# Optimization experiments

Measured on AMD Instinct MI355X. Metric: run time of the kernel, lower is better.

Reference implementation:

```python
import jax, jax.numpy as jnp
import numpy as np

B, Q, PAST, MAXC = 2, 1024, 1024, 4096
H, HKV, D, HID = 32, 8, 128, 4096
HALF = D // 2
GROUPS = H // HKV
EPS = 1e-6
SCALE = 1.0 / (D ** 0.5)


def setup_inputs() -> dict:
    key = jax.random.key(0)
    ks = jax.random.split(key, 6)
    hidden_states = jax.random.normal(ks[0], (B, Q, HID), jnp.float32)
    k_cache = jax.random.normal(ks[1], (B, HKV, MAXC, D), jnp.float32)
    v_cache = jax.random.normal(ks[2], (B, HKV, MAXC, D), jnp.float32)
    # rope table: [1, max_pos, head_dim], cos in first half, sin in second half
    inv_freq = 1.0 / (10000.0 ** (jnp.arange(0, HALF, dtype=jnp.float32) / HALF))
    ang = jnp.arange(MAXC, dtype=jnp.float32)[:, None] * inv_freq[None, :]
    rope_rotary_cos_sin = jnp.concatenate([jnp.cos(ang), jnp.sin(ang)], axis=-1)[None]
    context_lengths = jnp.full((B,), Q, dtype=jnp.int32)
    kvcache_start_index = jnp.full((B,), PAST, dtype=jnp.int32)
    w_qkv = jax.random.normal(ks[3], (HID, (H + 2 * HKV) * D), jnp.float32) * 0.02
    w_o = jax.random.normal(ks[4], (HKV * D, HID), jnp.float32) * 0.02
    q_norm_w = jnp.ones((D,), jnp.float32)
    k_norm_w = jnp.ones((D,), jnp.float32)
    return dict(hidden_states=hidden_states, k_cache=k_cache, v_cache=v_cache,
                rope_rotary_cos_sin=rope_rotary_cos_sin,
                context_lengths=context_lengths,
                kvcache_start_index=kvcache_start_index,
                w_qkv=w_qkv, w_o=w_o, q_norm_w=q_norm_w, k_norm_w=k_norm_w)


def _rms_norm(x, w):
    # x: [..., D]; per-head RMSNorm as in EdgeLLMQKNorm
    var = jnp.mean(x * x, axis=-1, keepdims=True)
    return x * jax.lax.rsqrt(var + EPS) * w


def _apply_rope(x, cos, sin):
    # x: [B, h, Q, D]; cos/sin: [B, Q, HALF] gathered by position_ids
    c = cos[:, None, :, :]
    s = sin[:, None, :, :]
    x1, x2 = x[..., :HALF], x[..., HALF:]
    return jnp.concatenate([x1 * c - x2 * s, x2 * c + x1 * s], axis=-1)


def _cache_update(cache, new, pos_ids):
    # cache: [B, HKV, MAXC, D]; new: [B, HKV, Q, D]; pos_ids: [B, Q]
    b_idx = jnp.arange(B)[:, None]  # [B,1]
    cache_t = jnp.swapaxes(cache, 1, 2)          # [B, MAXC, HKV, D]
    new_t = jnp.swapaxes(new, 1, 2)              # [B, Q, HKV, D]
    cache_t = cache_t.at[b_idx, pos_ids].set(new_t)
    return jnp.swapaxes(cache_t, 1, 2)


def reference(hidden_states, k_cache, v_cache, rope_rotary_cos_sin,
              context_lengths, kvcache_start_index, w_qkv, w_o,
              q_norm_w, k_norm_w):
    bsz, q_len, _ = hidden_states.shape
    # fused QKV projection
    qkv = jnp.einsum('bqh,hd->bqd', hidden_states, w_qkv)
    q, k, v = jnp.split(qkv, [H * D, (H + HKV) * D], axis=-1)
    # per-head QK norm (norm_shape = [B, Q, -1, head_dim])
    q = _rms_norm(q.reshape(bsz, q_len, H, D), q_norm_w)
    k = _rms_norm(k.reshape(bsz, q_len, HKV, D), k_norm_w)
    v = v.reshape(bsz, q_len, HKV, D)
    q = jnp.swapaxes(q, 1, 2)   # [B, H, Q, D]
    k = jnp.swapaxes(k, 1, 2)   # [B, HKV, Q, D]
    v = jnp.swapaxes(v, 1, 2)
    # rope tables (batch row 0), gather by position ids
    cos_t = rope_rotary_cos_sin[0, :, :HALF]  # [max_pos, HALF]
    sin_t = rope_rotary_cos_sin[0, :, HALF:]
    pos_ids = kvcache_start_index[:, None] + jnp.arange(q_len, dtype=jnp.int32)[None, :]  # [B,Q]
    cos = cos_t[pos_ids]
    sin = sin_t[pos_ids]
    q = _apply_rope(q, cos, sin)
    k = _apply_rope(k, cos, sin)
    # dynamic KV-cache write at kvcache_start_index
    present_k_cache = _cache_update(k_cache, k, pos_ids)
    present_v_cache = _cache_update(v_cache, v, pos_ids)
    present_length = PAST + Q  # = max(start) + max(context_lengths), static here
    k_present = present_k_cache[:, :, :present_length, :]
    v_present = present_v_cache[:, :, :present_length, :]
    # GQA head expansion
    k_exp = jnp.repeat(k_present, GROUPS, axis=1)   # [B, H, K, D]
    v_exp = jnp.repeat(v_present, GROUPS, axis=1)
    scores = jnp.einsum('bhqd,bhkd->bhqk', q * SCALE, k_exp)
    seq_k = present_length
    offset = seq_k - q_len
    causal = (jnp.arange(seq_k)[None, :] > (jnp.arange(q_len)[:, None] + offset))
    scores = jnp.where(causal[None, None], -jnp.inf, scores)
    attn = jax.nn.softmax(scores, axis=-1)
    out = jnp.einsum('bhqk,bhkd->bhqd', attn, v_exp)  # [B, H, Q, D]
    # norm is None & H > HKV: sum over GQA group dim (faithful to source)
    out = out.reshape(bsz, HKV, GROUPS, q_len, D).sum(axis=2)  # [B, HKV, Q, D]
    out = jnp.swapaxes(out, 1, 2).reshape(bsz, q_len, HKV * D)
    attn_output = jnp.einsum('bqd,dh->bqh', out, w_o)  # [B, Q, HID]
    return attn_output, present_k_cache, present_v_cache
```

## Files before the change

### kernel.cpp

```cpp
#include <hip/hip_runtime.h>


typedef __bf16 bf16;
typedef __attribute__((ext_vector_type(8))) __bf16 bf16x8;
typedef __attribute__((ext_vector_type(4))) __bf16 bf16x4;
typedef __attribute__((ext_vector_type(4))) float f32x4;
typedef __attribute__((ext_vector_type(4))) unsigned int u32x4;

#define NB 2
#define NQ 1024
#define PAST 1024
#define MAXC 4096
#define NH 32
#define NKV 8
#define HD 128
#define HID 4096
#define SEQK 2048
#define QKV_N 6144
#define SCALE 0.08838834764831845f
#define LOG2E 1.4426950408889634f
#define QSCALE (0.08838834764831845f * 1.4426950408889634f)

__device__ __forceinline__ void async16(const bf16* g, bf16* l) {
    __builtin_amdgcn_global_load_lds(
        (const __attribute__((address_space(1))) void*)g,
        (__attribute__((address_space(3))) void*)l, 16, 0, 0);
}

__global__ __launch_bounds__(512, 2) void gemm_qkv(const bf16* __restrict__ A,
                                                   const bf16* __restrict__ Bt,
                                                   bf16* __restrict__ C,
                                                   int N, int K) {
    __shared__ bf16 As[2][256 * 64];
    __shared__ bf16 Bs[2][192 * 64];
    const int orig = blockIdx.x;
    const int wg   = (orig & 7) * 32 + (orig >> 3);
    const int by   = wg & 7, bx = wg >> 3;
    const int rowBase = by * 256, colBase = bx * 192;

    const int tid  = threadIdx.x;
    const int lane = tid & 63;
    const int wv   = tid >> 6;
    const int wm   = wv >> 2, wn = wv & 3;
    const int l15  = lane & 15, quad = lane >> 4;

    const int sr = lane >> 3;
    const int sc = ((lane & 7) ^ sr) * 8;
    const bf16* aG = A  + (long)(rowBase + wv * 32 + sr) * K + sc;
    const bf16* bG = Bt + (long)(colBase + wv * 24 + sr) * K + sc;

    f32x4 acc[8][3];
#pragma unroll
    for (int i = 0; i < 8; i++)
#pragma unroll
        for (int j = 0; j < 3; j++) acc[i][j] = (f32x4){0.f, 0.f, 0.f, 0.f};

    const int nt = K >> 6;
#pragma unroll
    for (int j = 0; j < 4; j++)
        async16(aG + (long)(j * 8) * K, &As[0][(wv * 32 + j * 8) * 64]);
#pragma unroll
    for (int j = 0; j < 3; j++)
        async16(bG + (long)(j * 8) * K, &Bs[0][(wv * 24 + j * 8) * 64]);
    __syncthreads();

    for (int t = 0; t < nt; t++) {
        const int cur = t & 1;
        if (t + 1 < nt) {
            const int kn = (t + 1) << 6;
#pragma unroll
            for (int j = 0; j < 4; j++)
                async16(aG + (long)(j * 8) * K + kn, &As[cur ^ 1][(wv * 32 + j * 8) * 64]);
#pragma unroll
            for (int j = 0; j < 3; j++)
                async16(bG + (long)(j * 8) * K + kn, &Bs[cur ^ 1][(wv * 24 + j * 8) * 64]);
        }
#pragma unroll
        for (int kc = 0; kc < 2; kc++) {
            bf16x8 af[8], bfr[3];
#pragma unroll
            for (int mi = 0; mi < 8; mi++)
                af[mi] = *(const bf16x8*)&As[cur][(wm * 128 + mi * 16 + l15) * 64 +
                                                  ((kc * 32 + quad * 8) ^ ((l15 & 7) * 8))];
#pragma unroll
            for (int ni = 0; ni < 3; ni++)
                bfr[ni] = *(const bf16x8*)&Bs[cur][(wn * 48 + ni * 16 + l15) * 64 +
                                                   ((kc * 32 + quad * 8) ^ ((l15 & 7) * 8))];
            __builtin_amdgcn_s_setprio(1);
#pragma unroll
            for (int mi = 0; mi < 8; mi++)
#pragma unroll
                for (int ni = 0; ni < 3; ni++)
                    acc[mi][ni] = __builtin_amdgcn_mfma_f32_16x16x32_bf16(
                        af[mi], bfr[ni], acc[mi][ni], 0, 0, 0);
            __builtin_amdgcn_s_setprio(0);
        }
        __syncthreads();
    }
#pragma unroll
    for (int mi = 0; mi < 8; mi++)
#pragma unroll
        for (int r = 0; r < 4; r++) {
            const int row = rowBase + wm * 128 + mi * 16 + quad * 4 + r;
#pragma unroll
            for (int ni = 0; ni < 3; ni++) {
                const int col = colBase + wn * 48 + ni * 16 + l15;
                C[(long)row * N + col] = (bf16)acc[mi][ni][r];
            }
        }
}

template <bool F32OUT>
__global__ __launch_bounds__(256) void gemm_bb(const bf16* __restrict__ A,
                                               const bf16* __restrict__ Bt,
                                               void* __restrict__ Cv,
                                               int M, int N, int K, int nbx) {
    __shared__ bf16 As[2][128 * 64];
    __shared__ bf16 Bs[2][128 * 64];
    const int nwg  = gridDim.x;
    const int cpx  = nwg >> 3;
    const int orig = blockIdx.x;
    const int wg   = (orig & 7) * cpx + (orig >> 3);
    const int by = wg / nbx, bx = wg - by * nbx;
    const int rowBase = by * 128, colBase = bx * 128;

    const int tid  = threadIdx.x;
    const int lane = tid & 63;
    const int wv   = tid >> 6;
    const int wm   = wv >> 1, wn = wv & 1;
    const int l15  = lane & 15, quad = lane >> 4;

    const int sr = lane >> 3;
    const int sc = ((lane & 7) ^ sr) * 8;
    const bf16* aG = A  + (long)(rowBase + wv * 32 + sr) * K + sc;
    const bf16* bG = Bt + (long)(colBase + wv * 32 + sr) * K + sc;

    f32x4 acc[4][4];
#pragma unroll
    for (int i = 0; i < 4; i++)
#pragma unroll
        for (int j = 0; j < 4; j++) acc[i][j] = (f32x4){0.f, 0.f, 0.f, 0.f};

    const int nt = K >> 6;
#pragma unroll
    for (int j = 0; j < 4; j++) {
        async16(aG + (long)(j * 8) * K, &As[0][(wv * 32 + j * 8) * 64]);
        async16(bG + (long)(j * 8) * K, &Bs[0][(wv * 32 + j * 8) * 64]);
    }
    __syncthreads();

    for (int t = 0; t < nt; t++) {
        const int cur = t & 1;
        if (t + 1 < nt) {
            const int kn = (t + 1) << 6;
#pragma unroll
            for (int j = 0; j < 4; j++) {
                async16(aG + (long)(j * 8) * K + kn, &As[cur ^ 1][(wv * 32 + j * 8) * 64]);
                async16(bG + (long)(j * 8) * K + kn, &Bs[cur ^ 1][(wv * 32 + j * 8) * 64]);
            }
        }
#pragma unroll
        for (int kc = 0; kc < 2; kc++) {
            bf16x8 af[4], bfr[4];
#pragma unroll
            for (int mi = 0; mi < 4; mi++)
                af[mi] = *(const bf16x8*)&As[cur][(wm * 64 + mi * 16 + l15) * 64 +
                                                  ((kc * 32 + quad * 8) ^ ((l15 & 7) * 8))];
#pragma unroll
            for (int ni = 0; ni < 4; ni++)
                bfr[ni] = *(const bf16x8*)&Bs[cur][(wn * 64 + ni * 16 + l15) * 64 +
                                                   ((kc * 32 + quad * 8) ^ ((l15 & 7) * 8))];
            __builtin_amdgcn_s_setprio(1);
#pragma unroll
            for (int mi = 0; mi < 4; mi++)
#pragma unroll
                for (int ni = 0; ni < 4; ni++)
                    acc[mi][ni] = __builtin_amdgcn_mfma_f32_16x16x32_bf16(
                        af[mi], bfr[ni], acc[mi][ni], 0, 0, 0);
            __builtin_amdgcn_s_setprio(0);
        }
        __syncthreads();
    }
#pragma unroll
    for (int mi = 0; mi < 4; mi++)
#pragma unroll
        for (int r = 0; r < 4; r++) {
            const int row = rowBase + wm * 64 + mi * 16 + quad * 4 + r;
#pragma unroll
            for (int ni = 0; ni < 4; ni++) {
                const int col = colBase + wn * 64 + ni * 16 + l15;
                if (F32OUT) ((float*)Cv)[(long)row * N + col] = acc[mi][ni][r];
                else        ((bf16*)Cv)[(long)row * N + col] = (bf16)acc[mi][ni][r];
            }
        }
}

__global__ void conv_f2b(const float* __restrict__ in, bf16* __restrict__ out) {
    const long e = ((long)blockIdx.x * 256 + threadIdx.x) * 8;
    const f32x4 a = *(const f32x4*)&in[e];
    const f32x4 b = *(const f32x4*)&in[e + 4];
    bf16x8 v;
#pragma unroll
    for (int j = 0; j < 4; j++) { v[j] = (bf16)a[j]; v[4 + j] = (bf16)b[j]; }
    *(bf16x8*)&out[e] = v;
}

__global__ __launch_bounds__(256) void transpose_f2b(const float* __restrict__ in,
                                                     bf16* __restrict__ out,
                                                     int R, int C) {
    __shared__ bf16 t[64][72];
    const int r0 = blockIdx.y * 64, c0 = blockIdx.x * 64;
    const int tid = threadIdx.x;
    const int lr = tid >> 3;
    const int lc = (tid & 7) * 8;
#pragma unroll
    for (int i = 0; i < 2; i++) {
        const f32x4* p = (const f32x4*)&in[(long)(r0 + lr + i * 32) * C + c0 + lc];
        const f32x4 v0 = p[0], v1 = p[1];
        bf16x8 v;
#pragma unroll
        for (int j = 0; j < 4; j++) { v[j] = (bf16)v0[j]; v[4 + j] = (bf16)v1[j]; }
        *(bf16x8*)&t[lr + i * 32][lc] = v;
    }
    __syncthreads();
#pragma unroll
    for (int i = 0; i < 2; i++) {
        const int oc = lr + i * 32;
        bf16x8 v;
#pragma unroll
        for (int j = 0; j < 8; j++) v[j] = t[lc + j][oc];
        *(bf16x8*)&out[(long)(c0 + oc) * R + r0 + lc] = v;
    }
}

__global__ __launch_bounds__(256) void transpose_bf16(const bf16* __restrict__ in,
                                                      bf16* __restrict__ out,
                                                      int R, int C,
                                                      long inBS, long outBS) {
    __shared__ bf16 t[64][72];
    in  += (long)blockIdx.z * inBS;
    out += (long)blockIdx.z * outBS;
    const int r0 = blockIdx.y * 64, c0 = blockIdx.x * 64;
    const int tid = threadIdx.x;
    const int lr = tid >> 3;
    const int lc = (tid & 7) * 8;
#pragma unroll
    for (int i = 0; i < 2; i++)
        *(u32x4*)&t[lr + i * 32][lc] =
            *(const u32x4*)&in[(long)(r0 + lr + i * 32) * C + c0 + lc];
    __syncthreads();
#pragma unroll
    for (int i = 0; i < 2; i++) {
        const int oc = lr + i * 32;
        bf16x8 v;
#pragma unroll
        for (int j = 0; j < 8; j++) v[j] = t[lc + j][oc];
        *(bf16x8*)&out[(long)(c0 + oc) * R + r0 + lc] = v;
    }
}

__global__ void cache_to_bf16(const float* __restrict__ kc, const float* __restrict__ vc,
                              bf16* __restrict__ kb, bf16* __restrict__ vb) {
    const int bh = blockIdx.y;
    const long idx = ((long)blockIdx.x * 256 + threadIdx.x) * 8;
    const float* src = (blockIdx.z ? vc : kc) + (long)bh * MAXC * HD + idx;
    bf16* dst = (blockIdx.z ? vb : kb) + (long)bh * SEQK * HD + idx;
    const f32x4 a = *(const f32x4*)src;
    const f32x4 b = *(const f32x4*)(src + 4);
    bf16x8 v;
#pragma unroll
    for (int j = 0; j < 4; j++) { v[j] = (bf16)a[j]; v[4 + j] = (bf16)b[j]; }
    *(bf16x8*)dst = v;
}

__global__ void qkv_post(const bf16* __restrict__ qkv, const float* __restrict__ cs,
                         const int* __restrict__ kvstart,
                         const float* __restrict__ qw, const float* __restrict__ kw,
                         bf16* __restrict__ qbuf, float* __restrict__ outk,
                         float* __restrict__ outv, bf16* __restrict__ kb,
                         bf16* __restrict__ vb) {
    const int h = blockIdx.x;
    const int q = blockIdx.y;
    const int b = blockIdx.z;
    const int l = threadIdx.x;
    const bf16* x = qkv + (long)(b * NQ + q) * QKV_N + h * HD;
    float x1 = (float)x[l], x2 = (float)x[l + 64];
    const int pos = kvstart[b] + q;
    if (h < 40) {
        float sq = x1 * x1 + x2 * x2;
#pragma unroll
        for (int m = 32; m >= 1; m >>= 1) sq += __shfl_xor(sq, m);
        const float rr = rsqrtf(sq * (1.0f / 128.0f) + 1e-6f);
        const float w1 = (h < 32) ? qw[l] : kw[l];
        const float w2 = (h < 32) ? qw[l + 64] : kw[l + 64];
        const float y1 = x1 * rr * w1;
        const float y2 = x2 * rr * w2;
        const float c = cs[(long)pos * HD + l];
        const float s = cs[(long)pos * HD + 64 + l];
        const float o1 = y1 * c - y2 * s;
        const float o2 = y2 * c + y1 * s;
        if (h < 32) {
            bf16* dst = qbuf + ((long)(b * NH + h) * NQ + q) * HD;
            dst[l] = (bf16)(o1 * QSCALE);
            dst[l + 64] = (bf16)(o2 * QSCALE);
        } else {
            const int hk = h - 32;
            float* df = outk + ((long)(b * NKV + hk) * MAXC + pos) * HD;
            df[l] = o1; df[l + 64] = o2;
            bf16* db = kb + ((long)(b * NKV + hk) * SEQK + pos) * HD;
            db[l] = (bf16)o1; db[l + 64] = (bf16)o2;
        }
    } else {
        const int hk = h - 40;
        float* df = outv + ((long)(b * NKV + hk) * MAXC + pos) * HD;
        df[l] = x1; df[l + 64] = x2;
        bf16* db = vb + ((long)(b * NKV + hk) * SEQK + pos) * HD;
        db[l] = (bf16)x1; db[l + 64] = (bf16)x2;
    }
}

__global__ __launch_bounds__(256, 2) void attn_fwd(const bf16* __restrict__ qbuf,
                                                   const bf16* __restrict__ kb,
                                                   const bf16* __restrict__ vt,
                                                   bf16* __restrict__ oheads) {
    const int ib  = blockIdx.x + 8 * (blockIdx.y + 32 * blockIdx.z);
    const int xc  = ib & 7, j = ib >> 3;
    const int g   = xc * 8 + (j & 7);
    const int h   = g & 31, b = g >> 5;
    const int qraw = j >> 3;
    const int qt  = (qraw < 4) ? qraw : 11 - qraw;
    const int hk  = h >> 2;
    const int tid = threadIdx.x;
    const int lane = tid & 63, wv = tid >> 6;
    const int l15 = lane & 15, quad = lane >> 4;

    __shared__ bf16 Ks[2][64][128];
    __shared__ bf16 Vs[2][128][64];
    __shared__ bf16 Ps[4][32][64];

    const int qb = qt * 128 + wv * 32;

    bf16x8 aq[2][4];
#pragma unroll
    for (int ss = 0; ss < 2; ss++) {
        const bf16* qp = qbuf + ((long)(b * NH + h) * NQ + qb + ss * 16 + l15) * HD + quad * 8;
#pragma unroll
        for (int kc = 0; kc < 4; kc++) aq[ss][kc] = *(const bf16x8*)(qp + kc * 32);
    }

    f32x4 o[2][8];
    float m_[2], l_[2];
#pragma unroll
    for (int ss = 0; ss < 2; ss++) {
#pragma unroll
        for (int dt = 0; dt < 8; dt++) o[ss][dt] = (f32x4){0.f, 0.f, 0.f, 0.f};
        m_[ss] = -1e30f; l_[ss] = 0.f;
    }

    const long kcb = (long)(b * NKV + hk) * SEQK * HD;
    const long vtb = (long)(b * NKV + hk) * HD * (long)SEQK;
    const int ntiles = (qt * 128 + 127 + PAST + 64) >> 6;

    u32x4 kreg[4], vreg[4];
#pragma unroll
    for (int i = 0; i < 4; i++) {
        const int c = tid + i * 256;
        kreg[i] = *(const u32x4*)&kb[kcb + (long)(c >> 4) * HD + (c & 15) * 8];
        vreg[i] = *(const u32x4*)&vt[vtb + (long)(c >> 3) * SEQK + (c & 7) * 8];
    }
#pragma unroll
    for (int i = 0; i < 4; i++) {
        const int c = tid + i * 256;
        const int kr = c >> 4, kc8 = (c & 15) * 8;
        *(u32x4*)&Ks[0][kr][kc8 ^ ((kr & 7) * 8)] = kreg[i];
        const int vr = c >> 3, vc8 = (c & 7) * 8;
        *(u32x4*)&Vs[0][vr][vc8 ^ ((vr & 7) * 8)] = vreg[i];
    }
#pragma unroll
    for (int i = 0; i < 4; i++) {
        const int c = tid + i * 256;
        kreg[i] = *(const u32x4*)&kb[kcb + (long)(64 + (c >> 4)) * HD + (c & 15) * 8];
        vreg[i] = *(const u32x4*)&vt[vtb + (long)(c >> 3) * SEQK + 64 + (c & 7) * 8];
    }
    __syncthreads();

    for (int t = 0; t < ntiles; t++) {
        const int cur = t & 1;
        const int k0 = t * 64;
        if (t + 1 < ntiles) {
#pragma unroll
            for (int i = 0; i < 4; i++) {
                const int c = tid + i * 256;
                const int kr = c >> 4, kc8 = (c & 15) * 8;
                *(u32x4*)&Ks[cur ^ 1][kr][kc8 ^ ((kr & 7) * 8)] = kreg[i];
                const int vr = c >> 3, vc8 = (c & 7) * 8;
                *(u32x4*)&Vs[cur ^ 1][vr][vc8 ^ ((vr & 7) * 8)] = vreg[i];
            }
        }
        if (t + 2 < ntiles) {
            const int k0n = k0 + 128;
#pragma unroll
            for (int i = 0; i < 4; i++) {
                const int c = tid + i * 256;
                kreg[i] = *(const u32x4*)&kb[kcb + (long)(k0n + (c >> 4)) * HD + (c & 15) * 8];
                vreg[i] = *(const u32x4*)&vt[vtb + (long)(c >> 3) * SEQK + k0n + (c & 7) * 8];
            }
        }

#pragma unroll
        for (int ss = 0; ss < 2; ss++) {
            const int rbase = qb + ss * 16;
            if (k0 > rbase + 15 + PAST) continue;
            f32x4 s[4];
#pragma unroll
            for (int nk = 0; nk < 4; nk++) s[nk] = (f32x4){0.f, 0.f, 0.f, 0.f};
            __builtin_amdgcn_s_setprio(1);
#pragma unroll
            for (int kc = 0; kc < 4; kc++)
#pragma unroll
                for (int nk = 0; nk < 4; nk++) {
                    const bf16x8 bk = *(const bf16x8*)
                        &Ks[cur][nk * 16 + l15][(kc * 32 + quad * 8) ^ ((l15 & 7) * 8)];
                    s[nk] = __builtin_amdgcn_mfma_f32_16x16x32_bf16(bk, aq[ss][kc], s[nk], 0, 0, 0);
                }
            __builtin_amdgcn_s_setprio(0);
            if (k0 + 63 > rbase + PAST) {
                const int lim = rbase + l15 + PAST - k0;
#pragma unroll
                for (int nk = 0; nk < 4; nk++)
#pragma unroll
                    for (int r = 0; r < 4; r++)
                        if (nk * 16 + quad * 4 + r > lim) s[nk][r] = -1e30f;
            }
            float mx = s[0][0];
#pragma unroll
            for (int nk = 0; nk < 4; nk++)
#pragma unroll
                for (int r = 0; r < 4; r++) mx = fmaxf(mx, s[nk][r]);
            mx = fmaxf(mx, __shfl_xor(mx, 16));
            mx = fmaxf(mx, __shfl_xor(mx, 32));
            const float mn = fmaxf(m_[ss], mx);
            const float alpha = exp2f(m_[ss] - mn);
            float sum = 0.f;
#pragma unroll
            for (int nk = 0; nk < 4; nk++)
#pragma unroll
                for (int r = 0; r < 4; r++) {
                    const float p = exp2f(s[nk][r] - mn);
                    s[nk][r] = p;
                    sum += p;
                }
            sum += __shfl_xor(sum, 16);
            sum += __shfl_xor(sum, 32);
            l_[ss] = l_[ss] * alpha + sum;
            m_[ss] = mn;
#pragma unroll
            for (int nk = 0; nk < 4; nk++) {
                bf16x4 pv;
#pragma unroll
                for (int r = 0; r < 4; r++) pv[r] = (bf16)s[nk][r];
                *(bf16x4*)&Ps[wv][ss * 16 + l15][(nk * 16 + quad * 4) ^ ((l15 & 7) * 8)] = pv;
            }
#pragma unroll
            for (int r = 0; r < 4; r++) {
                const float ar = __shfl(alpha, (lane & 48) + quad * 4 + r);
#pragma unroll
                for (int dt = 0; dt < 8; dt++) o[ss][dt][r] *= ar;
            }
        }
#pragma unroll
        for (int ss = 0; ss < 2; ss++) {
            const int rbase = qb + ss * 16;
            if (k0 > rbase + 15 + PAST) continue;
            __builtin_amdgcn_s_setprio(1);
#pragma unroll
            for (int kc = 0; kc < 2; kc++) {
                const bf16x8 ap = *(const bf16x8*)
                    &Ps[wv][ss * 16 + l15][(kc * 32 + quad * 8) ^ ((l15 & 7) * 8)];
#pragma unroll
                for (int dt = 0; dt < 8; dt++) {
                    const bf16x8 bv = *(const bf16x8*)
                        &Vs[cur][dt * 16 + l15][(kc * 32 + quad * 8) ^ ((l15 & 7) * 8)];
                    o[ss][dt] = __builtin_amdgcn_mfma_f32_16x16x32_bf16(ap, bv, o[ss][dt], 0, 0, 0);
                }
            }
            __builtin_amdgcn_s_setprio(0);
        }
        __syncthreads();
    }

#pragma unroll
    for (int ss = 0; ss < 2; ss++) {
        float inv[4];
#pragma unroll
        for (int r = 0; r < 4; r++) {
            const float lr = __shfl(l_[ss], (lane & 48) + quad * 4 + r);
            inv[r] = 1.0f / lr;
        }
#pragma unroll
        for (int dt = 0; dt < 8; dt++)
#pragma unroll
            for (int r = 0; r < 4; r++) {
                const int row = qb + ss * 16 + quad * 4 + r;
                oheads[((long)(b * NH + h) * NQ + row) * HD + dt * 16 + l15] =
                    (bf16)(o[ss][dt][r] * inv[r]);
            }
    }
}

__global__ void group_sum(const bf16* __restrict__ oheads, bf16* __restrict__ osum) {
    const long e = ((long)blockIdx.x * 256 + threadIdx.x) * 8;
    const int b = (int)(e >> 20);
    const int rem = (int)(e & 1048575);
    const int q = rem >> 10;
    const int col = rem & 1023;
    const int hk = col >> 7;
    const int d = col & 127;
    float acc[8] = {0.f, 0.f, 0.f, 0.f, 0.f, 0.f, 0.f, 0.f};
#pragma unroll
    for (int g = 0; g < 4; g++) {
        const bf16x8 v = *(const bf16x8*)
            &oheads[((long)(b * NH + hk * 4 + g) * NQ + q) * HD + d];
#pragma unroll
        for (int j = 0; j < 8; j++) acc[j] += (float)v[j];
    }
    bf16x8 r;
#pragma unroll
    for (int j = 0; j < 8; j++) r[j] = (bf16)acc[j];
    *(bf16x8*)&osum[e] = r;
}

extern "C" void kernel_launch(void* const* d_in, const int* in_sizes, int n_in,
                              void* d_out, int out_size, void* d_ws, size_t ws_size,
                              hipStream_t stream) {
    const float* hidden  = (const float*)d_in[0];
    const float* kc_in   = (const float*)d_in[1];
    const float* vc_in   = (const float*)d_in[2];
    const float* rope_cs = (const float*)d_in[3];
    const int*   kvstart = (const int*)d_in[5];
    const float* w_qkv   = (const float*)d_in[6];
    const float* w_o     = (const float*)d_in[7];
    const float* qnw     = (const float*)d_in[8];
    const float* knw     = (const float*)d_in[9];

    float* out_attn = (float*)d_out;
    float* out_k    = out_attn + 8388608L;
    float* out_v    = out_k + 8388608L;

    char* ob = (char*)d_out;
    bf16* qbuf  = (bf16*)ob;
    bf16* kb16  = (bf16*)(ob + 16777216);
    bf16* vtb16 = (bf16*)(ob + 25165824);
    bf16* wqkvT = (bf16*)(ob + 33554432);
    bf16* hb16  = (bf16*)(ob + 83886080);

    char* ws = (char*)d_ws;
    bf16*  qkvb   = (bf16*)ws;
    bf16*  vpb16  = (bf16*)(ws + 25165824);
    bf16*  oheads = (bf16*)ws;
    bf16*  osum   = (bf16*)(ws + 16777216);
    bf16*  woT    = (bf16*)(ws + 25165824);

    conv_f2b<<<dim3(4096), 256, 0, stream>>>(hidden, hb16);
    transpose_f2b<<<dim3(96, 64), 256, 0, stream>>>(w_qkv, wqkvT, HID, QKV_N);
    gemm_qkv<<<dim3(256), 512, 0, stream>>>(hb16, wqkvT, qkvb, QKV_N, HID);
    hipMemcpyAsync(out_k, kc_in, 33554432, hipMemcpyDeviceToDevice, stream);
    hipMemcpyAsync(out_v, vc_in, 33554432, hipMemcpyDeviceToDevice, stream);
    cache_to_bf16<<<dim3(128, 16, 2), 256, 0, stream>>>(kc_in, vc_in, kb16, vpb16);
    qkv_post<<<dim3(48, NQ, NB), 64, 0, stream>>>(qkvb, rope_cs, kvstart, qnw, knw,
                                                  qbuf, out_k, out_v, kb16, vpb16);
    transpose_bf16<<<dim3(2, 32, 16), 256, 0, stream>>>(vpb16, vtb16, SEQK, HD,
                                                        (long)SEQK * HD, (long)SEQK * HD);
    attn_fwd<<<dim3(8, NH, NB), 256, 0, stream>>>(qbuf, kb16, vtb16, oheads);
    group_sum<<<dim3(1024), 256, 0, stream>>>(oheads, osum);
    transpose_f2b<<<dim3(64, 16), 256, 0, stream>>>(w_o, woT, 1024, HID);
    gemm_bb<true><<<dim3(512), 256, 0, stream>>>(osum, woT, out_attn, 2048, HID, 1024, 32);
}
```

Before: 527.9 us.

## Load K/V directly from global per wave, drop LDS staging and block syncs

Removes the shared-memory double-buffered K/V tiles and the per-tile block barrier. Each wave now reads K and V fragments straight from global memory (relying on L2/cache), with a per-wave tile count. It also shares each K/V fragment across both 16-row sub-tiles, skips the rescale of the running max unless it grows by more than 8 (lazy rescale), and raises occupancy to 3 blocks per CU. The trade-off is redundant global traffic across the four waves and uncached, possibly poorly coalesced loads in exchange for no LDS stores and no syncs.

```diff
diff --git a/kernel.cpp b/kernel.cpp
--- a/kernel.cpp
+++ b/kernel.cpp
@@ -319,7 +319,7 @@
     }
 }
 
-__global__ __launch_bounds__(256, 2) void attn_fwd(const bf16* __restrict__ qbuf,
+__global__ __launch_bounds__(256, 3) void attn_fwd(const bf16* __restrict__ qbuf,
                                                    const bf16* __restrict__ kb,
                                                    const bf16* __restrict__ vt,
                                                    bf16* __restrict__ oheads) {
@@ -334,8 +334,6 @@
     const int lane = tid & 63, wv = tid >> 6;
     const int l15 = lane & 15, quad = lane >> 4;
 
-    __shared__ bf16 Ks[2][64][128];
-    __shared__ bf16 Vs[2][128][64];
     __shared__ bf16 Ps[4][32][64];
 
     const int qb = qt * 128 + wv * 32;
@@ -357,136 +355,103 @@
         m_[ss] = -1e30f; l_[ss] = 0.f;
     }
 
-    const long kcb = (long)(b * NKV + hk) * SEQK * HD;
-    const long vtb = (long)(b * NKV + hk) * HD * (long)SEQK;
-    const int ntiles = (qt * 128 + 127 + PAST + 64) >> 6;
-
-    u32x4 kreg[4], vreg[4];
-#pragma unroll
-    for (int i = 0; i < 4; i++) {
-        const int c = tid + i * 256;
-        kreg[i] = *(const u32x4*)&kb[kcb + (long)(c >> 4) * HD + (c & 15) * 8];
-        vreg[i] = *(const u32x4*)&vt[vtb + (long)(c >> 3) * SEQK + (c & 7) * 8];
-    }
-#pragma unroll
-    for (int i = 0; i < 4; i++) {
-        const int c = tid + i * 256;
-        const int kr = c >> 4, kc8 = (c & 15) * 8;
-        *(u32x4*)&Ks[0][kr][kc8 ^ ((kr & 7) * 8)] = kreg[i];
-        const int vr = c >> 3, vc8 = (c & 7) * 8;
-        *(u32x4*)&Vs[0][vr][vc8 ^ ((vr & 7) * 8)] = vreg[i];
-    }
-#pragma unroll
-    for (int i = 0; i < 4; i++) {
-        const int c = tid + i * 256;
-        kreg[i] = *(const u32x4*)&kb[kcb + (long)(64 + (c >> 4)) * HD + (c & 15) * 8];
-        vreg[i] = *(const u32x4*)&vt[vtb + (long)(c >> 3) * SEQK + 64 + (c & 7) * 8];
-    }
-    __syncthreads();
+    const bf16* kB = kb + (long)(b * NKV + hk) * SEQK * HD;
+    const bf16* vB = vt + (long)(b * NKV + hk) * HD * (long)SEQK;
+
+    const int lastk  = qb + 31 + PAST;
+    const int ntiles = (lastk >> 6) + 1;
 
     for (int t = 0; t < ntiles; t++) {
-        const int cur = t & 1;
         const int k0 = t * 64;
-        if (t + 1 < ntiles) {
-#pragma unroll
-            for (int i = 0; i < 4; i++) {
-                const int c = tid + i * 256;
-                const int kr = c >> 4, kc8 = (c & 15) * 8;
-                *(u32x4*)&Ks[cur ^ 1][kr][kc8 ^ ((kr & 7) * 8)] = kreg[i];
-                const int vr = c >> 3, vc8 = (c & 7) * 8;
-                *(u32x4*)&Vs[cur ^ 1][vr][vc8 ^ ((vr & 7) * 8)] = vreg[i];
-            }
-        }
-        if (t + 2 < ntiles) {
-            const int k0n = k0 + 128;
-#pragma unroll
-            for (int i = 0; i < 4; i++) {
-                const int c = tid + i * 256;
-                kreg[i] = *(const u32x4*)&kb[kcb + (long)(k0n + (c >> 4)) * HD + (c & 15) * 8];
-                vreg[i] = *(const u32x4*)&vt[vtb + (long)(c >> 3) * SEQK + k0n + (c & 7) * 8];
-            }
-        }
+
+        f32x4 s[2][4];
+#pragma unroll
+        for (int nk = 0; nk < 4; nk++) {
+            s[0][nk] = (f32x4){0.f, 0.f, 0.f, 0.f};
+            s[1][nk] = (f32x4){0.f, 0.f, 0.f, 0.f};
+        }
+        __builtin_amdgcn_s_setprio(1);
+#pragma unroll
+        for (int kc = 0; kc < 4; kc++) {
+            bf16x8 bk[4];
+#pragma unroll
+            for (int nk = 0; nk < 4; nk++)
+                bk[nk] = *(const bf16x8*)&kB[(long)(k0 + nk * 16 + l15) * HD + kc * 32 + quad * 8];
+#pragma unroll
+            for (int nk = 0; nk < 4; nk++) {
+                s[0][nk] = __builtin_amdgcn_mfma_f32_16x16x32_bf16(bk[nk], aq[0][kc], s[0][nk], 0, 0, 0);
+                s[1][nk] = __builtin_amdgcn_mfma_f32_16x16x32_bf16(bk[nk], aq[1][kc], s[1][nk], 0, 0, 0);
+            }
+        }
+        __builtin_amdgcn_s_setprio(0);
 
 #pragma unroll
         for (int ss = 0; ss < 2; ss++) {
             const int rbase = qb + ss * 16;
-            if (k0 > rbase + 15 + PAST) continue;
-            f32x4 s[4];
-#pragma unroll
-            for (int nk = 0; nk < 4; nk++) s[nk] = (f32x4){0.f, 0.f, 0.f, 0.f};
-            __builtin_amdgcn_s_setprio(1);
-#pragma unroll
-            for (int kc = 0; kc < 4; kc++)
-#pragma unroll
-                for (int nk = 0; nk < 4; nk++) {
-                    const bf16x8 bk = *(const bf16x8*)
-                        &Ks[cur][nk * 16 + l15][(kc * 32 + quad * 8) ^ ((l15 & 7) * 8)];
-                    s[nk] = __builtin_amdgcn_mfma_f32_16x16x32_bf16(bk, aq[ss][kc], s[nk], 0, 0, 0);
-                }
-            __builtin_amdgcn_s_setprio(0);
             if (k0 + 63 > rbase + PAST) {
                 const int lim = rbase + l15 + PAST - k0;
 #pragma unroll
                 for (int nk = 0; nk < 4; nk++)
 #pragma unroll
                     for (int r = 0; r < 4; r++)
-                        if (nk * 16 + quad * 4 + r > lim) s[nk][r] = -1e30f;
-            }
-            float mx = s[0][0];
+                        if (nk * 16 + quad * 4 + r > lim) s[ss][nk][r] = -1e30f;
+            }
+            float mx = s[ss][0][0];
 #pragma unroll
             for (int nk = 0; nk < 4; nk++)
 #pragma unroll
-                for (int r = 0; r < 4; r++) mx = fmaxf(mx, s[nk][r]);
+                for (int r = 0; r < 4; r++) mx = fmaxf(mx, s[ss][nk][r]);
             mx = fmaxf(mx, __shfl_xor(mx, 16));
             mx = fmaxf(mx, __shfl_xor(mx, 32));
-            const float mn = fmaxf(m_[ss], mx);
-            const float alpha = exp2f(m_[ss] - mn);
+            if (!__all(mx - m_[ss] <= 8.f)) {
+                const float mn = fmaxf(m_[ss], mx);
+                const float alpha = exp2f(m_[ss] - mn);
+                m_[ss] = mn;
+                l_[ss] *= alpha;
+#pragma unroll
+                for (int r = 0; r < 4; r++) {
+                    const float ar = __shfl(alpha, (lane & 48) + quad * 4 + r);
+#pragma unroll
+                    for (int dt = 0; dt < 8; dt++) o[ss][dt][r] *= ar;
+                }
+            }
             float sum = 0.f;
 #pragma unroll
             for (int nk = 0; nk < 4; nk++)
 #pragma unroll
                 for (int r = 0; r < 4; r++) {
-                    const float p = exp2f(s[nk][r] - mn);
-                    s[nk][r] = p;
+                    const float p = exp2f(s[ss][nk][r] - m_[ss]);
+                    s[ss][nk][r] = p;
                     sum += p;
                 }
             sum += __shfl_xor(sum, 16);
             sum += __shfl_xor(sum, 32);
-            l_[ss] = l_[ss] * alpha + sum;
-            m_[ss] = mn;
+            l_[ss] += sum;
 #pragma unroll
             for (int nk = 0; nk < 4; nk++) {
                 bf16x4 pv;
 #pragma unroll
-                for (int r = 0; r < 4; r++) pv[r] = (bf16)s[nk][r];
+                for (int r = 0; r < 4; r++) pv[r] = (bf16)s[ss][nk][r];
                 *(bf16x4*)&Ps[wv][ss * 16 + l15][(nk * 16 + quad * 4) ^ ((l15 & 7) * 8)] = pv;
             }
-#pragma unroll
-            for (int r = 0; r < 4; r++) {
-                const float ar = __shfl(alpha, (lane & 48) + quad * 4 + r);
-#pragma unroll
-                for (int dt = 0; dt < 8; dt++) o[ss][dt][r] *= ar;
-            }
-        }
-#pragma unroll
-        for (int ss = 0; ss < 2; ss++) {
-            const int rbase = qb + ss * 16;
-            if (k0 > rbase + 15 + PAST) continue;
-            __builtin_amdgcn_s_setprio(1);
-#pragma unroll
-            for (int kc = 0; kc < 2; kc++) {
-                const bf16x8 ap = *(const bf16x8*)
-                    &Ps[wv][ss * 16 + l15][(kc * 32 + quad * 8) ^ ((l15 & 7) * 8)];
-#pragma unroll
-                for (int dt = 0; dt < 8; dt++) {
-                    const bf16x8 bv = *(const bf16x8*)
-                        &Vs[cur][dt * 16 + l15][(kc * 32 + quad * 8) ^ ((l15 & 7) * 8)];
-                    o[ss][dt] = __builtin_amdgcn_mfma_f32_16x16x32_bf16(ap, bv, o[ss][dt], 0, 0, 0);
-                }
-            }
-            __builtin_amdgcn_s_setprio(0);
-        }
-        __syncthreads();
+        }
+
+        __builtin_amdgcn_s_setprio(1);
+#pragma unroll
+        for (int kc = 0; kc < 2; kc++) {
+            const bf16x8 ap0 = *(const bf16x8*)
+                &Ps[wv][l15][(kc * 32 + quad * 8) ^ ((l15 & 7) * 8)];
+            const bf16x8 ap1 = *(const bf16x8*)
+                &Ps[wv][16 + l15][(kc * 32 + quad * 8) ^ ((l15 & 7) * 8)];
+#pragma unroll
+            for (int dt = 0; dt < 8; dt++) {
+                const bf16x8 bv = *(const bf16x8*)
+                    &vB[(long)(dt * 16 + l15) * SEQK + k0 + kc * 32 + quad * 8];
+                o[0][dt] = __builtin_amdgcn_mfma_f32_16x16x32_bf16(ap0, bv, o[0][dt], 0, 0, 0);
+                o[1][dt] = __builtin_amdgcn_mfma_f32_16x16x32_bf16(ap1, bv, o[1][dt], 0, 0, 0);
+            }
+        }
+        __builtin_amdgcn_s_setprio(0);
     }
 
 #pragma unroll
```

Measured after the change: 765.8 us. 1.45x slower.
